# Kernel optimization log

Hardware: AMD Instinct MI355X
Metric: run time of the kernel (lower is better)

The kernel has to match this reference:

```python
import jax, jax.numpy as jnp
import numpy as np
from jax import lax

DN = ('NCH', 'OIH', 'NCH')

def conv1d(x, w, b, pad=0):
    y = lax.conv_general_dilated(x, w, window_strides=(1,), padding=[(pad, pad)], dimension_numbers=DN)
    return y + b[None, :, None]

def conv_transpose1d(x, w_torch, b):
    # torch ConvTranspose1d weight: [C_in, C_out, K]; equivalent to full conv with flipped kernel
    k = w_torch.shape[-1]
    w = jnp.flip(jnp.transpose(w_torch, (1, 0, 2)), axis=-1)  # [C_out, C_in, K]
    y = lax.conv_general_dilated(x, w, window_strides=(1,), padding=[(k - 1, k - 1)], dimension_numbers=DN)
    return y + b[None, :, None]

def converter(signal, w1, b1, w2, b2, wt, bt, w3, b3):
    h = jax.nn.relu(conv1d(signal, w1, b1))          # [B,10,n-2]
    h = jax.nn.relu(conv1d(h, w2, b2))               # [B,10,n-2]
    h = jax.nn.relu(conv_transpose1d(h, wt, bt))     # [B,10,n]
    h = jax.nn.sigmoid(conv1d(h, w3, b3))            # [B,2,n]
    return h

def setup_inputs() -> dict:
    key = jax.random.key(0)
    ks = jax.random.split(key, 12)
    B, C, n = 32, 128, 8192
    signal = jax.random.normal(ks[0], (B, C, n), dtype=jnp.float32)
    curr_diag = jax.random.uniform(ks[1], (B, n - 1), dtype=jnp.float32) + 0.5
    s = 0.1
    return {
        'signal': signal,
        'curr_diag': curr_diag,
        'index_diag': 1,
        'w1': jax.random.normal(ks[2], (10, C, 3), dtype=jnp.float32) * s,
        'b1': jax.random.normal(ks[3], (10,), dtype=jnp.float32) * s,
        'w2': jax.random.normal(ks[4], (10, 10, 1), dtype=jnp.float32) * s,
        'b2': jax.random.normal(ks[5], (10,), dtype=jnp.float32) * s,
        'wt': jax.random.normal(ks[6], (10, 10, 3), dtype=jnp.float32) * s,
        'bt': jax.random.normal(ks[7], (10,), dtype=jnp.float32) * s,
        'w3': jax.random.normal(ks[8], (2, 10, 1), dtype=jnp.float32) * s,
        'b3': jax.random.normal(ks[9], (2,), dtype=jnp.float32) * s,
        'const': jnp.float32(0.99),
    }

def reference(signal, curr_diag, index_diag, w1, b1, w2, b2, wt, bt, w3, b3, const):
    n = signal.shape[-1]
    lr = converter(signal, w1, b1, w2, b2, wt, bt, w3, b3)  # [B,2,n]
    left, right = lr[:, 0, :], lr[:, 1, :]
    # diag_len = n - index_diag; next diag has length diag_len - 1
    mass_in = curr_diag[:, 1:] * right[:, 1:n - index_diag]
    mass_in = mass_in + curr_diag[:, :-1] * left[:, index_diag:n - 1]
    mass_out = right[:, 0:n - index_diag - 1] + left[:, index_diag + 1:n]
    next_diag = const * mass_in / mass_out
    next_diag = jnp.log(next_diag)
    next_diag = next_diag - jnp.mean(next_diag)
    return next_diag
```

## Files before the change

### kernel.cpp

```cpp
#include <hip/hip_runtime.h>
#include <math.h>

#define B     32
#define CIN   128
#define NN    8192
#define N1    8190
#define CH    10
#define TOUT  252
#define NTILE 33
#define COLS  264
#define CPC   8
#define NCHK  16

__global__ void k0_prep(const float* __restrict__ w1, float* __restrict__ wT)
{
    const int i = blockIdx.x * 256 + threadIdx.x;
    if (i < CIN * 32) {
        const int ci = i >> 5, r = i & 31;
        float v = 0.f;
        if (r < 30) {
            const int o = r / 3, k = r - o * 3;
            v = w1[(o * CIN + ci) * 3 + k];
        }
        wT[i] = v;
    }
}

typedef __attribute__((address_space(1))) void g_void;
typedef __attribute__((address_space(3))) void l_void;

__device__ __forceinline__ void gld16(const float* g, float* l)
{
    __builtin_amdgcn_global_load_lds((g_void*)g, (l_void*)l, 16, 0, 0);
}

__device__ __forceinline__ void stage_chunk(const float* __restrict__ sigb, int c,
                                            float* buf, int tid, int scol0)
{
    const float* rowbase = sigb + (size_t)(c * CPC) * NN;
#pragma unroll
    for (int k = 0; k < 2; ++k) {
        const int i = k * 256 + tid;
        const int row = (int)((unsigned)i / 66u);
        int col = scol0 + (i - row * 66) * 4;
        col = col < 0 ? 0 : (col > NN - 4 ? NN - 4 : col);
        gld16(rowbase + (size_t)row * NN + col, buf + i * 4);
    }
    if (tid < 16) {
        const int i = 512 + tid;
        int col = scol0 + (i - 462) * 4;
        col = col > NN - 4 ? NN - 4 : col;
        gld16(rowbase + (size_t)7 * NN + col, buf + i * 4);
    }
}

__global__ __launch_bounds__(256, 4) void k_main(
    const float* __restrict__ sig, const float* __restrict__ wT,
    const float* __restrict__ b1, const float* __restrict__ w2, const float* __restrict__ b2,
    const float* __restrict__ wt, const float* __restrict__ bt,
    const float* __restrict__ w3, const float* __restrict__ b3,
    const float* __restrict__ cd, const float* __restrict__ cstp,
    float* __restrict__ outv, float* __restrict__ bsums)
{
    __shared__ float bufA[CPC * COLS];
    __shared__ float bufB[CPC * COLS];
    __shared__ float h2s[CH * 256];
    __shared__ float lsh[256], rsh[256];
    __shared__ float red[4];

    const int tid = threadIdx.x;
    const int b   = blockIdx.y;
    const int t0  = blockIdx.x * TOUT;
    const int scol0 = t0 - 4;
    const int g   = t0 - 2 + tid;
    const bool gvalid = (g >= 0) && (g < N1);
    const float* __restrict__ sigb = sig + (size_t)b * CIN * NN;

    float y[CH];
#pragma unroll
    for (int o = 0; o < CH; ++o) y[o] = b1[o];

    stage_chunk(sigb, 0, bufA, tid, scol0);
    __syncthreads();

    for (int c = 0; c < NCHK; ++c) {
        float* cur = (c & 1) ? bufB : bufA;
        float* nxt = (c & 1) ? bufA : bufB;
        if (c < NCHK - 1) stage_chunk(sigb, c + 1, nxt, tid, scol0);

        const float* bl = cur + tid + 2;
#pragma unroll
        for (int j = 0; j < CPC; ++j) {
            const float s0 = bl[j * COLS + 0];
            const float s1 = bl[j * COLS + 1];
            const float s2 = bl[j * COLS + 2];
            const float* wrow = wT + (c * CPC + j) * 32;
#pragma unroll
            for (int o = 0; o < CH; ++o) {
                y[o] = fmaf(wrow[o * 3 + 0], s0, y[o]);
                y[o] = fmaf(wrow[o * 3 + 1], s1, y[o]);
                y[o] = fmaf(wrow[o * 3 + 2], s2, y[o]);
            }
        }
        __syncthreads();
    }

#pragma unroll
    for (int o = 0; o < CH; ++o) y[o] = fmaxf(y[o], 0.f);
#pragma unroll
    for (int o = 0; o < CH; ++o) {
        float a = b2[o];
#pragma unroll
        for (int i = 0; i < CH; ++i) a = fmaf(w2[o * CH + i], y[i], a);
        h2s[o * 256 + tid] = gvalid ? fmaxf(a, 0.f) : 0.f;
    }
    __syncthreads();

    const int s = t0 + tid;
    if (tid < 254 && s < NN) {
        float acc[CH];
#pragma unroll
        for (int o = 0; o < CH; ++o) acc[o] = bt[o];
#pragma unroll
        for (int i = 0; i < CH; ++i) {
            const float a0 = h2s[i * 256 + tid];
            const float a1 = h2s[i * 256 + tid + 1];
            const float a2 = h2s[i * 256 + tid + 2];
            const float* wp = wt + i * CH * 3;
#pragma unroll
            for (int o = 0; o < CH; ++o) {
                acc[o] = fmaf(wp[o * 3 + 0], a2, acc[o]);
                acc[o] = fmaf(wp[o * 3 + 1], a1, acc[o]);
                acc[o] = fmaf(wp[o * 3 + 2], a0, acc[o]);
            }
        }
        float l = b3[0], r = b3[1];
#pragma unroll
        for (int o = 0; o < CH; ++o) {
            const float h3 = fmaxf(acc[o], 0.f);
            l = fmaf(w3[o],      h3, l);
            r = fmaf(w3[CH + o], h3, r);
        }
        lsh[tid] = 1.f / (1.f + __expf(-l));
        rsh[tid] = 1.f / (1.f + __expf(-r));
    }
    __syncthreads();

    float vlog = 0.f;
    const int t = t0 + tid;
    if (tid < TOUT && t < N1) {
        const float c0 = cd[(size_t)b * (NN - 1) + t];
        const float c1 = cd[(size_t)b * (NN - 1) + t + 1];
        const float mi = c1 * rsh[tid + 1] + c0 * lsh[tid + 1];
        const float mo = rsh[tid] + lsh[tid + 2];
        vlog = __logf(cstp[0] * mi / mo);
        outv[(size_t)b * N1 + t] = vlog;
    }

    float vs = vlog;
#pragma unroll
    for (int off = 32; off > 0; off >>= 1) vs += __shfl_down(vs, off);
    if ((tid & 63) == 0) red[tid >> 6] = vs;
    __syncthreads();
    if (tid == 0)
        bsums[blockIdx.y * NTILE + blockIdx.x] = red[0] + red[1] + red[2] + red[3];
}

__global__ __launch_bounds__(256) void k3_meansub(
    const float* __restrict__ bsums, float* __restrict__ outv, int n)
{
    __shared__ float red[256];
    const int tid = threadIdx.x;
    float s = 0.f;
    for (int i = tid; i < NTILE * B; i += 256) s += bsums[i];
    red[tid] = s;
    __syncthreads();
#pragma unroll
    for (int st = 128; st > 0; st >>= 1) {
        if (tid < st) red[tid] += red[tid + st];
        __syncthreads();
    }
    const float mean = red[0] / (float)(B * N1);
    __syncthreads();
    const int i = blockIdx.x * 256 + tid;
    if (i < n) outv[i] -= mean;
}

extern "C" void kernel_launch(void* const* d_in, const int* in_sizes, int n_in,
                              void* d_out, int out_size, void* d_ws, size_t ws_size,
                              hipStream_t stream)
{
    const float* sig = (const float*)d_in[0];
    const float* cd  = (const float*)d_in[1];
    const float* w1  = (const float*)d_in[3];
    const float* b1  = (const float*)d_in[4];
    const float* w2  = (const float*)d_in[5];
    const float* b2  = (const float*)d_in[6];
    const float* wt  = (const float*)d_in[7];
    const float* bt  = (const float*)d_in[8];
    const float* w3  = (const float*)d_in[9];
    const float* b3  = (const float*)d_in[10];
    const float* cst = (const float*)d_in[11];

    float* outv = (float*)d_out;

    float* ws   = (float*)d_ws;
    float* wT   = ws;
    float* bsum = wT + CIN * 32;

    k0_prep   <<<dim3(16), dim3(256), 0, stream>>>(w1, wT);
    k_main    <<<dim3(NTILE, B), dim3(256), 0, stream>>>(sig, wT, b1, w2, b2,
                                                         wt, bt, w3, b3, cd, cst, outv, bsum);
    k3_meansub<<<dim3((out_size + 255) / 256), dim3(256), 0, stream>>>(bsum, outv, out_size);
}
```

Measured before the change: 239.6 us.

## Triple-buffer signal staging with explicit vmcnt waits and per-wave loads

```diff
diff --git a/kernel.cpp b/kernel.cpp
--- a/kernel.cpp
+++ b/kernel.cpp
@@ -34,23 +34,47 @@
     __builtin_amdgcn_global_load_lds((g_void*)g, (l_void*)l, 16, 0, 0);
 }
 
-__device__ __forceinline__ void stage_chunk(const float* __restrict__ sigb, int c,
-                                            float* buf, int tid, int scol0)
+#define WAITVM(N) asm volatile("s_waitcnt vmcnt(" #N ")" ::: "memory")
+#define BARRIER() asm volatile("s_barrier" ::: "memory")
+#define BAR_RD()  asm volatile("s_waitcnt lgkmcnt(0)\n\ts_barrier" ::: "memory")
+
+__device__ __forceinline__ void stage_one(const float* __restrict__ rowbase,
+                                          float* buf, int i, int scol0)
+{
+    const int row = (int)((unsigned)i / 66u);
+    int col = scol0 + (i - row * 66) * 4;
+    col = col < 0 ? 0 : (col > NN - 4 ? NN - 4 : col);
+    gld16(rowbase + (size_t)row * NN + col, buf + (size_t)i * 4);
+}
+
+__device__ __forceinline__ void stage3(const float* __restrict__ sigb, int c,
+                                       float* buf, int wav, int lane, int scol0)
 {
     const float* rowbase = sigb + (size_t)(c * CPC) * NN;
-#pragma unroll
-    for (int k = 0; k < 2; ++k) {
-        const int i = k * 256 + tid;
-        const int row = (int)((unsigned)i / 66u);
-        int col = scol0 + (i - row * 66) * 4;
-        col = col < 0 ? 0 : (col > NN - 4 ? NN - 4 : col);
-        gld16(rowbase + (size_t)row * NN + col, buf + i * 4);
-    }
-    if (tid < 16) {
-        const int i = 512 + tid;
-        int col = scol0 + (i - 462) * 4;
-        col = col > NN - 4 ? NN - 4 : col;
-        gld16(rowbase + (size_t)7 * NN + col, buf + i * 4);
+    const int base = wav * 132;
+    stage_one(rowbase, buf, base + lane, scol0);
+    stage_one(rowbase, buf, base + 64 + lane, scol0);
+    if (lane < 4)
+        stage_one(rowbase, buf, base + 128 + lane, scol0);
+}
+
+__device__ __forceinline__ void chunkfma(const float* __restrict__ cur, int c,
+                                         int tid, float (&y)[CH],
+                                         const float* __restrict__ wT)
+{
+    const float* bl = cur + tid + 2;
+#pragma unroll
+    for (int j = 0; j < CPC; ++j) {
+        const float s0 = bl[j * COLS + 0];
+        const float s1 = bl[j * COLS + 1];
+        const float s2 = bl[j * COLS + 2];
+        const float* wrow = wT + (c * CPC + j) * 32;
+#pragma unroll
+        for (int o = 0; o < CH; ++o) {
+            y[o] = fmaf(wrow[o * 3 + 0], s0, y[o]);
+            y[o] = fmaf(wrow[o * 3 + 1], s1, y[o]);
+            y[o] = fmaf(wrow[o * 3 + 2], s2, y[o]);
+        }
     }
 }
 
@@ -64,15 +88,18 @@
 {
     __shared__ float bufA[CPC * COLS];
     __shared__ float bufB[CPC * COLS];
+    __shared__ float bufC[CPC * COLS];
     __shared__ float h2s[CH * 256];
     __shared__ float lsh[256], rsh[256];
     __shared__ float red[4];
 
-    const int tid = threadIdx.x;
-    const int b   = blockIdx.y;
-    const int t0  = blockIdx.x * TOUT;
+    const int tid  = threadIdx.x;
+    const int wav  = tid >> 6;
+    const int lane = tid & 63;
+    const int b    = blockIdx.y;
+    const int t0   = blockIdx.x * TOUT;
     const int scol0 = t0 - 4;
-    const int g   = t0 - 2 + tid;
+    const int g    = t0 - 2 + tid;
     const bool gvalid = (g >= 0) && (g < N1);
     const float* __restrict__ sigb = sig + (size_t)b * CIN * NN;
 
@@ -80,30 +107,27 @@
 #pragma unroll
     for (int o = 0; o < CH; ++o) y[o] = b1[o];
 
-    stage_chunk(sigb, 0, bufA, tid, scol0);
-    __syncthreads();
-
-    for (int c = 0; c < NCHK; ++c) {
-        float* cur = (c & 1) ? bufB : bufA;
-        float* nxt = (c & 1) ? bufA : bufB;
-        if (c < NCHK - 1) stage_chunk(sigb, c + 1, nxt, tid, scol0);
-
-        const float* bl = cur + tid + 2;
-#pragma unroll
-        for (int j = 0; j < CPC; ++j) {
-            const float s0 = bl[j * COLS + 0];
-            const float s1 = bl[j * COLS + 1];
-            const float s2 = bl[j * COLS + 2];
-            const float* wrow = wT + (c * CPC + j) * 32;
-#pragma unroll
-            for (int o = 0; o < CH; ++o) {
-                y[o] = fmaf(wrow[o * 3 + 0], s0, y[o]);
-                y[o] = fmaf(wrow[o * 3 + 1], s1, y[o]);
-                y[o] = fmaf(wrow[o * 3 + 2], s2, y[o]);
-            }
-        }
-        __syncthreads();
-    }
+    stage3(sigb, 0, bufA, wav, lane, scol0);
+    __builtin_amdgcn_sched_barrier(0);
+    stage3(sigb, 1, bufB, wav, lane, scol0);
+    __builtin_amdgcn_sched_barrier(0);
+    stage3(sigb, 2, bufC, wav, lane, scol0);
+    __syncthreads();
+
+    float* p0 = bufA; float* p1 = bufB; float* p2 = bufC;
+    for (int c = 0; c < 13; ++c) {
+        WAITVM(6);
+        BARRIER();
+        chunkfma(p0, c, tid, y, wT);
+        BAR_RD();
+        stage3(sigb, c + 3, p0, wav, lane, scol0);
+        float* t = p0; p0 = p1; p1 = p2; p2 = t;
+    }
+    WAITVM(6); BARRIER(); chunkfma(p0, 13, tid, y, wT);
+    { float* t = p0; p0 = p1; p1 = p2; p2 = t; }
+    WAITVM(3); BARRIER(); chunkfma(p0, 14, tid, y, wT);
+    { float* t = p0; p0 = p1; p1 = p2; p2 = t; }
+    WAITVM(0); BARRIER(); chunkfma(p0, 15, tid, y, wT);
 
 #pragma unroll
     for (int o = 0; o < CH; ++o) y[o] = fmaxf(y[o], 0.f);
```

New measurement: 305.7 us. 1.28x slower.
